# Performance work log

Hardware: AMD Instinct MI355X
Metric: run time of the kernel (lower is better)

The kernel has to match this reference:

```python
import jax, jax.numpy as jnp
import numpy as np

K = 20
EPS = 1e-5


def _bn(x, g, b):
    # inference-mode BatchNorm with running_mean=0, running_var=1 (fresh init)
    return x * (g / jnp.sqrt(1.0 + EPS)) + b


def _lrelu(x):
    return jax.nn.leaky_relu(x, 0.2)


def _knn(x, k):
    # x: [B,N,D] -> idx [B,N,k] of nearest neighbors (includes self)
    sq = jnp.sum(x * x, axis=-1)                       # [B,N]
    inner = jnp.einsum('bnd,bmd->bnm', x, x)           # [B,N,N]
    dist = sq[:, :, None] - 2.0 * inner + sq[:, None, :]
    _, idx = jax.lax.top_k(-dist, k)
    return idx


def _edge_feat(x, k):
    # x: [B,N,D] -> [B,N,k,2D] = concat(neighbor - center, center)
    idx = _knn(x, k)
    nbr = jax.vmap(lambda xb, ib: xb[ib])(x, idx)      # [B,N,k,D]
    ctr = jnp.broadcast_to(x[:, :, None, :], nbr.shape)
    return jnp.concatenate([nbr - ctr, ctr], axis=-1)


def _edge_conv(x, W, g, b, k):
    # conv1x1 (no bias) + BN + LeakyReLU + max over neighbors
    f = _edge_feat(x, k)                               # [B,N,k,2D]
    h = jnp.einsum('bnkc,oc->bnko', f, W)
    return jnp.max(_lrelu(_bn(h, g, b)), axis=2)       # [B,N,out]


def setup_inputs() -> dict:
    key = jax.random.key(0)
    ks = jax.random.split(key, 12)
    B, N = 8, 4096
    num_classes = 5
    r = lambda k_, shape: jax.random.normal(k_, shape, jnp.float32) * 0.1
    return {
        'xyz': jax.random.normal(ks[0], (B, N, 3), jnp.float32),
        'W1': r(ks[1], (64, 6)),   'g1': jnp.ones((64,), jnp.float32),  'b1': jnp.zeros((64,), jnp.float32),
        'W2': r(ks[2], (64, 128)), 'g2': jnp.ones((64,), jnp.float32),  'b2': jnp.zeros((64,), jnp.float32),
        'W3': r(ks[3], (64, 128)), 'g3': jnp.ones((64,), jnp.float32),  'b3': jnp.zeros((64,), jnp.float32),
        'W4': r(ks[4], (128, 128)),'g4': jnp.ones((128,), jnp.float32), 'b4': jnp.zeros((128,), jnp.float32),
        'W5': r(ks[5], (1024, 320)),'g5': jnp.ones((1024,), jnp.float32),'b5': jnp.zeros((1024,), jnp.float32),
        'Wl1': r(ks[6], (512, 2048)),'g6': jnp.ones((512,), jnp.float32),'b6': jnp.zeros((512,), jnp.float32),
        'Wl2': r(ks[7], (256, 512)), 'bl2': jnp.zeros((256,), jnp.float32),
        'g7': jnp.ones((256,), jnp.float32), 'b7': jnp.zeros((256,), jnp.float32),
        'Wl3': r(ks[8], (num_classes, 256)), 'bl3': jnp.zeros((num_classes,), jnp.float32),
    }


def reference(xyz, W1, g1, b1, W2, g2, b2, W3, g3, b3, W4, g4, b4,
              W5, g5, b5, Wl1, g6, b6, Wl2, bl2, g7, b7, Wl3, bl3):
    B, N, _ = xyz.shape
    k = min(K, N - 1)
    x1 = _edge_conv(xyz, W1, g1, b1, k)                # [B,N,64]
    x2 = _edge_conv(x1, W2, g2, b2, k)                 # [B,N,64]
    x3 = _edge_conv(x2, W3, g3, b3, k)                 # [B,N,64]
    x4 = _edge_conv(x3, W4, g4, b4, k)                 # [B,N,128]
    xc = jnp.concatenate([x1, x2, x3, x4], axis=-1)    # [B,N,320]
    h = _lrelu(_bn(jnp.einsum('bnc,oc->bno', xc, W5), g5, b5))  # [B,N,1024]
    gmax = jnp.max(h, axis=1)
    gavg = jnp.mean(h, axis=1)
    gfeat = jnp.concatenate([gmax, gavg], axis=-1)     # [B,2048]
    y = _lrelu(_bn(gfeat @ Wl1.T, g6, b6))             # dropout = identity (eval)
    y = _lrelu(_bn(y @ Wl2.T + bl2, g7, b7))
    y = y @ Wl3.T + bl3                                # [B,num_classes]
    return jnp.broadcast_to(y[:, None, :], (B, N, y.shape[-1]))
```

## Files before the change

kernel.cpp:

```cpp
#include <hip/hip_runtime.h>


constexpr int NB  = 8;
constexpr int NPT = 4096;
constexpr int KNB = 20;
constexpr int CAP = 128;

typedef _Float16 half8 __attribute__((ext_vector_type(8)));
typedef float f32x4 __attribute__((ext_vector_type(4)));

__device__ __forceinline__ unsigned int fmono(float f) {
  unsigned int u = __float_as_uint(f);
  return u ^ ((unsigned int)(((int)u) >> 31) | 0x80000000u);
}

__device__ __attribute__((noinline)) unsigned long long compact_row(
    int row, int n, int lane) {
  extern __shared__ char smem[];
  unsigned long long* buf = (unsigned long long*)smem + (size_t)row * CAP;
  const unsigned long long INFK = ~0ull;
  unsigned long long a = (lane < n) ? buf[lane] : INFK;
  unsigned long long c = (lane + 64 < n) ? buf[lane + 64] : INFK;
#pragma unroll
  for (int k = 2; k <= 64; k <<= 1) {
#pragma unroll
    for (int j = k >> 1; j > 0; j >>= 1) {
      const bool tm = (((lane & k) == 0) == ((lane & j) == 0));
      const unsigned long long oa = __shfl_xor(a, j, 64);
      a = ((a < oa) == tm) ? a : oa;
      const unsigned long long oc = __shfl_xor(c, j, 64);
      c = ((c < oc) == tm) ? oc : c;
    }
  }
  unsigned long long m = a < c ? a : c;
#pragma unroll
  for (int j = 32; j > 0; j >>= 1) {
    const unsigned long long o = __shfl_xor(m, j, 64);
    const bool low = (lane & j) == 0;
    m = ((m < o) == low) ? m : o;
  }
  return m;
}

__device__ __forceinline__ void sel4(unsigned long long k0,
                                     unsigned long long k1,
                                     unsigned long long k2,
                                     unsigned long long k3, int base_r,
                                     int quad, int lane, unsigned int below,
                                     unsigned long long& tau, int& cnt) {
  extern __shared__ char smem[];
  unsigned long long* bufB = (unsigned long long*)smem;
#pragma unroll 1
  for (int attempt = 0; attempt < 2; ++attempt) {
    const unsigned long long m0 = __ballot(k0 < tau);
    const unsigned long long m1 = __ballot(k1 < tau);
    const unsigned long long m2 = __ballot(k2 < tau);
    const unsigned long long m3 = __ballot(k3 < tau);
    if ((m0 | m1 | m2 | m3) == 0ull) return;
    const int sh = quad * 16;
    const unsigned int s0 = (unsigned int)(m0 >> sh) & 0xFFFFu;
    const unsigned int s1 = (unsigned int)(m1 >> sh) & 0xFFFFu;
    const unsigned int s2 = (unsigned int)(m2 >> sh) & 0xFFFFu;
    const unsigned int s3 = (unsigned int)(m3 >> sh) & 0xFFFFu;
    const int tot = __popc(s0) + __popc(s1) + __popc(s2) + __popc(s3);
    const unsigned long long needm = __ballot(cnt + tot > CAP);
    if (needm != 0ull && attempt == 0) {
#pragma unroll
      for (int q = 0; q < 4; ++q) {
        if ((needm >> (q * 16)) & 1ull) {
          const int nq = __shfl(cnt, q * 16, 64);
          const unsigned long long sv = compact_row(base_r + q * 4, nq, lane);
          const unsigned long long t19 = __shfl(sv, 19, 64);
          if (lane < 20) bufB[(size_t)(base_r + q * 4) * CAP + lane] = sv;
          if (quad == q) { tau = t19; cnt = 20; }
        }
      }
      continue;
    }
    int pos = cnt + __popc(s0 & below) + __popc(s1 & below) +
              __popc(s2 & below) + __popc(s3 & below);
    unsigned long long* bp = bufB + (size_t)(base_r + quad * 4) * CAP;
    if (k0 < tau) { bp[pos] = k0; ++pos; }
    if (k1 < tau) { bp[pos] = k1; ++pos; }
    if (k2 < tau) { bp[pos] = k2; ++pos; }
    if (k3 < tau) { bp[pos] = k3; }
    cnt += tot;
    return;
  }
}

__global__ __launch_bounds__(256) void cvt_xyz(const float* __restrict__ xyz,
                                               float* __restrict__ x0) {
  const int t = blockIdx.x * 256 + threadIdx.x;
  float4 v;
  v.x = xyz[t * 3 + 0];
  v.y = xyz[t * 3 + 1];
  v.z = xyz[t * 3 + 2];
  v.w = 0.0f;
  *(float4*)(x0 + (size_t)t * 4) = v;
}

__global__ __launch_bounds__(256) void sqsplit(const float* __restrict__ x,
                                               float* __restrict__ sqo,
                                               unsigned short* __restrict__ xhi,
                                               unsigned short* __restrict__ xlo) {
  const int t = blockIdx.x * 256 + threadIdx.x;
  const int p = t >> 2, c = t & 3;
  const float* src = x + (size_t)p * 64 + c * 16;
  float s = 0.0f;
  unsigned short hb[16], lb[16];
#pragma unroll
  for (int e = 0; e < 16; e += 4) {
    const float4 v = *(const float4*)(src + e);
    const float vv[4] = {v.x, v.y, v.z, v.w};
#pragma unroll
    for (int u = 0; u < 4; ++u) {
      const float f = vv[u];
      s = fmaf(f, f, s);
      const _Float16 h = (_Float16)f;
      const _Float16 l = (_Float16)(f - (float)h);
      hb[e + u] = __builtin_bit_cast(unsigned short, h);
      lb[e + u] = __builtin_bit_cast(unsigned short, l);
    }
  }
  unsigned short* dh = xhi + (size_t)p * 64 + c * 16;
  unsigned short* dl = xlo + (size_t)p * 64 + c * 16;
  *(uint4*)dh = *(uint4*)hb;
  *(uint4*)(dh + 8) = *(uint4*)(hb + 8);
  *(uint4*)dl = *(uint4*)lb;
  *(uint4*)(dl + 8) = *(uint4*)(lb + 8);
  s += __shfl_xor(s, 1, 64);
  s += __shfl_xor(s, 2, 64);
  if (c == 0) sqo[p] = s;
}

__global__ __launch_bounds__(256, 2) void knn3(const float* __restrict__ x0,
                                               int* __restrict__ idxout) {
  const int bid = blockIdx.x;
  const int b = bid & 7;
  const int i0 = (bid >> 3) * 64;
  const int tid = threadIdx.x, w = tid >> 6, lane = tid & 63;
  const int l15 = lane & 15, quad = lane >> 4;
  const unsigned int below = (1u << l15) - 1u;
  const float* xb = x0 + (size_t)b * (NPT * 4);

  float xix[4], xiy[4], xiz[4];
#pragma unroll
  for (int r = 0; r < 4; ++r) {
    const float4 v =
        *(const float4*)(xb + (size_t)(i0 + w * 16 + quad * 4 + r) * 4);
    xix[r] = v.x;
    xiy[r] = v.y;
    xiz[r] = v.z;
  }

  unsigned long long tau[4] = {~0ull, ~0ull, ~0ull, ~0ull};
  int cnt[4] = {0, 0, 0, 0};

  for (int jt = 0; jt < NPT / 64; ++jt) {
    const int j0 = jt * 64;
    float4 xj[4];
#pragma unroll
    for (int nj = 0; nj < 4; ++nj)
      xj[nj] = *(const float4*)(xb + (size_t)(j0 + nj * 16 + l15) * 4);
#pragma unroll
    for (int r = 0; r < 4; ++r) {
      unsigned long long k[4];
#pragma unroll
      for (int nj = 0; nj < 4; ++nj) {
        const float dx = xj[nj].x - xix[r];
        const float dy = xj[nj].y - xiy[r];
        const float dz = xj[nj].z - xiz[r];
        const float dd = fmaf(dx, dx, fmaf(dy, dy, dz * dz));
        k[nj] = ((unsigned long long)fmono(dd) << 32) |
                (unsigned int)(j0 + nj * 16 + l15);
      }
      sel4(k[0], k[1], k[2], k[3], w * 16 + r, quad, lane, below, tau[r],
           cnt[r]);
    }
  }
#pragma unroll 1
  for (int rw = 0; rw < 16; ++rw) {
    const int q = rw >> 2, r = rw & 3;
    const int nq = __shfl(cnt[r], q * 16, 64);
    const unsigned long long sv = compact_row(w * 16 + rw, nq, lane);
    const int i = i0 + w * 16 + rw;
    if (lane < 20)
      idxout[((size_t)(b * NPT + i)) * KNB + lane] = (int)(unsigned int)sv;
  }
}

__global__ __launch_bounds__(256, 2) void knn_mfma(
    const unsigned short* __restrict__ xhi16,
    const unsigned short* __restrict__ xlo16,
    const float* __restrict__ sqn, int* __restrict__ idxout) {
  const int bid = blockIdx.x;
  const int b = bid & 7;
  const int i0 = (bid >> 3) * 64;
  const int tid = threadIdx.x, w = tid >> 6, lane = tid & 63;
  const int l15 = lane & 15, quad = lane >> 4;
  const unsigned int below = (1u << l15) - 1u;

  const half8* Hb = (const half8*)(xhi16 + (size_t)b * NPT * 64);
  const half8* Lb = (const half8*)(xlo16 + (size_t)b * NPT * 64);
  const float* sqb = sqn + b * NPT;

  const int ia = i0 + w * 16 + l15;
  const half8 ah0 = Hb[(size_t)ia * 8 + quad];
  const half8 ah1 = Hb[(size_t)ia * 8 + 4 + quad];
  const half8 al0 = Lb[(size_t)ia * 8 + quad];
  const half8 al1 = Lb[(size_t)ia * 8 + 4 + quad];

  unsigned long long tau[4] = {~0ull, ~0ull, ~0ull, ~0ull};
  int cnt[4] = {0, 0, 0, 0};

  for (int jt = 0; jt < NPT / 64; ++jt) {
    const int j0 = jt * 64;
    float sq4[4];
#pragma unroll
    for (int nj = 0; nj < 4; ++nj) sq4[nj] = sqb[j0 + nj * 16 + l15];
    f32x4 acc[4];
#pragma unroll
    for (int nj = 0; nj < 4; ++nj) {
      const int jb = j0 + nj * 16 + l15;
      const half8 bh0 = Hb[(size_t)jb * 8 + quad];
      const half8 bh1 = Hb[(size_t)jb * 8 + 4 + quad];
      const half8 bl0 = Lb[(size_t)jb * 8 + quad];
      const half8 bl1 = Lb[(size_t)jb * 8 + 4 + quad];
      f32x4 a = {0.0f, 0.0f, 0.0f, 0.0f};
      a = __builtin_amdgcn_mfma_f32_16x16x32_f16(al0, bh0, a, 0, 0, 0);
      a = __builtin_amdgcn_mfma_f32_16x16x32_f16(al1, bh1, a, 0, 0, 0);
      a = __builtin_amdgcn_mfma_f32_16x16x32_f16(ah0, bl0, a, 0, 0, 0);
      a = __builtin_amdgcn_mfma_f32_16x16x32_f16(ah1, bl1, a, 0, 0, 0);
      a = __builtin_amdgcn_mfma_f32_16x16x32_f16(ah0, bh0, a, 0, 0, 0);
      a = __builtin_amdgcn_mfma_f32_16x16x32_f16(ah1, bh1, a, 0, 0, 0);
      acc[nj] = a;
    }
#pragma unroll
    for (int r = 0; r < 4; ++r) {
      unsigned long long k[4];
#pragma unroll
      for (int nj = 0; nj < 4; ++nj) {
        const float dd = fmaf(-2.0f, acc[nj][r], sq4[nj]);
        k[nj] = ((unsigned long long)fmono(dd) << 32) |
                (unsigned int)(j0 + nj * 16 + l15);
      }
      sel4(k[0], k[1], k[2], k[3], w * 16 + r, quad, lane, below, tau[r],
           cnt[r]);
    }
  }
#pragma unroll 1
  for (int rw = 0; rw < 16; ++rw) {
    const int q = rw >> 2, r = rw & 3;
    const int nq = __shfl(cnt[r], q * 16, 64);
    const unsigned long long sv = compact_row(w * 16 + rw, nq, lane);
    const int i = i0 + w * 16 + rw;
    if (lane < 20)
      idxout[((size_t)(b * NPT + i)) * KNB + lane] = (int)(unsigned int)sv;
  }
}

__global__ __launch_bounds__(256) void featg3(const float* __restrict__ x0,
                                              const float* __restrict__ W,
                                              float* __restrict__ Y) {
  const int lane = threadIdx.x & 63;
  const int p0 = (blockIdx.x * 4 + (threadIdx.x >> 6)) * 4;
  const float* wr = W + lane * 6;
  const float w0 = wr[0], w1 = wr[1], w2 = wr[2];
#pragma unroll
  for (int r = 0; r < 4; ++r) {
    const float4 v = *(const float4*)(x0 + (size_t)(p0 + r) * 4);
    Y[(size_t)(p0 + r) * 64 + lane] = w0 * v.x + w1 * v.y + w2 * v.z;
  }
}

__global__ __launch_bounds__(256) void featg64(const float* __restrict__ X,
                                               const float* __restrict__ W,
                                               int co, float* __restrict__ Y) {
  __shared__ float Xt[64][68];
  __shared__ float Wt[64][68];
  const int tid = threadIdx.x;
  const int n0 = blockIdx.x * 64;
  const int pc = tid & 63, dg = tid >> 6;
#pragma unroll
  for (int rep = 0; rep < 4; ++rep) {
    const int d0 = dg * 16 + rep * 4;
    const float4 xv = *(const float4*)(X + (size_t)(n0 + pc) * 64 + d0);
    Xt[d0 + 0][pc] = xv.x; Xt[d0 + 1][pc] = xv.y;
    Xt[d0 + 2][pc] = xv.z; Xt[d0 + 3][pc] = xv.w;
    const float4 wv = *(const float4*)(W + (size_t)(co + pc) * 128 + d0);
    Wt[d0 + 0][pc] = wv.x; Wt[d0 + 1][pc] = wv.y;
    Wt[d0 + 2][pc] = wv.z; Wt[d0 + 3][pc] = wv.w;
  }
  __syncthreads();
  const int c0 = (tid & 15) * 4, p0 = (tid >> 4) * 4;
  float acc[4][4];
#pragma unroll
  for (int i = 0; i < 4; ++i)
#pragma unroll
    for (int j = 0; j < 4; ++j) acc[i][j] = 0.0f;
#pragma unroll 4
  for (int d = 0; d < 64; ++d) {
    const float4 xa = *(const float4*)&Xt[d][p0];
    const float4 wc = *(const float4*)&Wt[d][c0];
    const float xr[4] = {xa.x, xa.y, xa.z, xa.w};
    const float wr[4] = {wc.x, wc.y, wc.z, wc.w};
#pragma unroll
    for (int i = 0; i < 4; ++i)
#pragma unroll
      for (int j = 0; j < 4; ++j) acc[i][j] = fmaf(xr[i], wr[j], acc[i][j]);
  }
#pragma unroll
  for (int i = 0; i < 4; ++i) {
    float4 o;
    o.x = acc[i][0]; o.y = acc[i][1]; o.z = acc[i][2]; o.w = acc[i][3];
    *(float4*)(Y + (size_t)(n0 + p0 + i) * 64 + c0) = o;
  }
}

template <int DIN, int DS, int COUT>
__global__ __launch_bounds__(256) void gather_edge(
    const float* __restrict__ x, const float* __restrict__ Y,
    const int* __restrict__ idx, const float* __restrict__ W,
    const float* __restrict__ g, const float* __restrict__ bia,
    float* __restrict__ out, int co) {
  const int lane = threadIdx.x & 63;
  const int wglob = blockIdx.x * 4 + (threadIdx.x >> 6);
  const int b = wglob >> 12;
  const int c = co + lane;

  const float* wrow = W + (size_t)c * (2 * DIN);
  const float* xi = x + (size_t)wglob * DS;
  float Dv = 0.0f;
  if constexpr (DIN == 3) {
    const float4 v = *(const float4*)xi;
    Dv = (wrow[3] - wrow[0]) * v.x + (wrow[4] - wrow[1]) * v.y +
         (wrow[5] - wrow[2]) * v.z;
  } else {
#pragma unroll
    for (int d0 = 0; d0 < DIN; d0 += 4) {
      const float4 wa4 = *(const float4*)(wrow + d0);
      const float4 wb4 = *(const float4*)(wrow + DIN + d0);
      const float4 v = *(const float4*)(xi + d0);
      Dv += (wb4.x - wa4.x) * v.x + (wb4.y - wa4.y) * v.y +
            (wb4.z - wa4.z) * v.z + (wb4.w - wa4.w) * v.w;
    }
  }
  const float invs = 1.0f / sqrtf(1.0f + 1e-5f);
  const float s = g[c] * invs;
  const float base = fmaf(s, Dv, bia[c]);

  const int* ip = idx + (size_t)wglob * KNB;
  const int jv = ip[lane < KNB ? lane : 0];
  const float* Yb = Y + (((size_t)b) << 12) * 64;
  float m = -3.0e38f;
#pragma unroll
  for (int k = 0; k < KNB; ++k) {
    const int j = __shfl(jv, k, 64);
    const float yv = Yb[(size_t)j * 64 + lane];
    float v = fmaf(s, yv, base);
    v = v > 0.0f ? v : 0.2f * v;
    m = fmaxf(m, v);
  }
  out[(size_t)wglob * COUT + c] = m;
}

__global__ __launch_bounds__(256) void conv5_kernel(
    const float* __restrict__ x1, const float* __restrict__ x2,
    const float* __restrict__ x3, const float* __restrict__ x4,
    const float* __restrict__ W5, const float* __restrict__ g5,
    const float* __restrict__ b5, float* __restrict__ pmax,
    float* __restrict__ psum) {
  __shared__ float xcT[320][32];
  __shared__ float wT[8][256];
  const int nb = blockIdx.x, cb = blockIdx.y, b = blockIdx.z;
  const int tid = threadIdx.x;
  const int n0 = nb * 32;

#pragma unroll
  for (int p = 0; p < 10; ++p) {
    const int q = tid + p * 256;
    const int nloc = q / 80;
    const int kg = (q % 80) * 4;
    const float* src;
    int koff;
    if (kg < 64)       { src = x1 + ((size_t)(b * NPT + n0 + nloc)) * 64;  koff = kg; }
    else if (kg < 128) { src = x2 + ((size_t)(b * NPT + n0 + nloc)) * 64;  koff = kg - 64; }
    else if (kg < 192) { src = x3 + ((size_t)(b * NPT + n0 + nloc)) * 64;  koff = kg - 128; }
    else               { src = x4 + ((size_t)(b * NPT + n0 + nloc)) * 128; koff = kg - 192; }
    const float4 v = *(const float4*)(src + koff);
    xcT[kg + 0][nloc] = v.x; xcT[kg + 1][nloc] = v.y;
    xcT[kg + 2][nloc] = v.z; xcT[kg + 3][nloc] = v.w;
  }

  const int cg = tid >> 2, ng = tid & 3;
  const int c0 = cg * 4, n0t = ng * 8;
  float acc[4][8];
#pragma unroll
  for (int r = 0; r < 4; ++r)
#pragma unroll
    for (int e = 0; e < 8; ++e) acc[r][e] = 0.0f;

  const float* wbase = W5 + (size_t)(cb * 256 + tid) * 320;
  float4 wA = *(const float4*)(wbase);
  float4 wB = *(const float4*)(wbase + 4);

  for (int kt = 0; kt < 40; ++kt) {
    __syncthreads();
    wT[0][tid] = wA.x; wT[1][tid] = wA.y; wT[2][tid] = wA.z; wT[3][tid] = wA.w;
    wT[4][tid] = wB.x; wT[5][tid] = wB.y; wT[6][tid] = wB.z; wT[7][tid] = wB.w;
    const int kn = (kt + 1 < 40) ? kt + 1 : 39;
    float4 nA = *(const float4*)(wbase + kn * 8);
    float4 nB = *(const float4*)(wbase + kn * 8 + 4);
    __syncthreads();
#pragma unroll
    for (int kk = 0; kk < 8; ++kk) {
      const float4 w4 = *(const float4*)&wT[kk][c0];
      const float4 xa = *(const float4*)&xcT[kt * 8 + kk][n0t];
      const float4 xb4 = *(const float4*)&xcT[kt * 8 + kk][n0t + 4];
      const float wr[4] = {w4.x, w4.y, w4.z, w4.w};
      const float xr[8] = {xa.x, xa.y, xa.z, xa.w, xb4.x, xb4.y, xb4.z, xb4.w};
#pragma unroll
      for (int r = 0; r < 4; ++r)
#pragma unroll
        for (int e = 0; e < 8; ++e) acc[r][e] = fmaf(wr[r], xr[e], acc[r][e]);
    }
    wA = nA; wB = nB;
  }

  const float invs = 1.0f / sqrtf(1.0f + 1e-5f);
#pragma unroll
  for (int r = 0; r < 4; ++r) {
    const int cglob = cb * 256 + c0 + r;
    const float s = g5[cglob] * invs;
    const float bb = b5[cglob];
    float mx = -3.0e38f, sm = 0.0f;
#pragma unroll
    for (int e = 0; e < 8; ++e) {
      float v = fmaf(s, acc[r][e], bb);
      v = v > 0.0f ? v : 0.2f * v;
      mx = fmaxf(mx, v);
      sm += v;
    }
    mx = fmaxf(mx, __shfl_xor(mx, 1, 64));
    mx = fmaxf(mx, __shfl_xor(mx, 2, 64));
    sm += __shfl_xor(sm, 1, 64);
    sm += __shfl_xor(sm, 2, 64);
    if (ng == 0) {
      pmax[((size_t)b * 1024 + cglob) * 128 + nb] = mx;
      psum[((size_t)b * 1024 + cglob) * 128 + nb] = sm;
    }
  }
}

__global__ __launch_bounds__(256) void reduce5(const float* __restrict__ pmax,
                                               const float* __restrict__ psum,
                                               float* __restrict__ gfeat) {
  const int t = blockIdx.x * 256 + threadIdx.x;
  const int b = t >> 10, c = t & 1023;
  const float* pm = pmax + (size_t)t * 128;
  const float* ps = psum + (size_t)t * 128;
  float mx = -3.0e38f, sm = 0.0f;
  for (int i = 0; i < 128; i += 4) {
    const float4 v = *(const float4*)(pm + i);
    mx = fmaxf(mx, fmaxf(fmaxf(v.x, v.y), fmaxf(v.z, v.w)));
    const float4 u = *(const float4*)(ps + i);
    sm += (u.x + u.y) + (u.z + u.w);
  }
  gfeat[b * 2048 + c] = mx;
  gfeat[b * 2048 + 1024 + c] = sm * (1.0f / 4096.0f);
}

__global__ __launch_bounds__(256) void head1(const float* __restrict__ gfeat,
                                             const float* __restrict__ Wl1,
                                             const float* __restrict__ g6,
                                             const float* __restrict__ b6,
                                             float* __restrict__ y1g) {
  __shared__ float gf[2048];
  __shared__ float red[256];
  const int tid = threadIdx.x;
  const int cb = blockIdx.x, b = blockIdx.y;
  const float4* gsrc = (const float4*)(gfeat + b * 2048);
  for (int p = tid; p < 512; p += 256) ((float4*)gf)[p] = gsrc[p];
  __syncthreads();
  const int cl = cb * 64 + (tid >> 2);
  const int q = tid & 3;
  const float* wr = Wl1 + (size_t)cl * 2048 + q * 512;
  const float* gq = gf + q * 512;
  float acc = 0.0f;
  for (int k0 = 0; k0 < 512; k0 += 8) {
    const float4 w0 = *(const float4*)(wr + k0);
    const float4 w1 = *(const float4*)(wr + k0 + 4);
    acc = fmaf(w0.x, gq[k0 + 0], acc); acc = fmaf(w0.y, gq[k0 + 1], acc);
    acc = fmaf(w0.z, gq[k0 + 2], acc); acc = fmaf(w0.w, gq[k0 + 3], acc);
    acc = fmaf(w1.x, gq[k0 + 4], acc); acc = fmaf(w1.y, gq[k0 + 5], acc);
    acc = fmaf(w1.z, gq[k0 + 6], acc); acc = fmaf(w1.w, gq[k0 + 7], acc);
  }
  red[tid] = acc;
  __syncthreads();
  if (q == 0) {
    float v = red[tid] + red[tid + 1] + red[tid + 2] + red[tid + 3];
    const float invs = 1.0f / sqrtf(1.0f + 1e-5f);
    v = fmaf(g6[cl] * invs, v, b6[cl]);
    v = v > 0.0f ? v : 0.2f * v;
    y1g[b * 512 + cl] = v;
  }
}

__global__ __launch_bounds__(256) void head2(
    const float* __restrict__ y1g, const float* __restrict__ Wl2,
    const float* __restrict__ bl2, const float* __restrict__ g7,
    const float* __restrict__ b7, const float* __restrict__ Wl3,
    const float* __restrict__ bl3, float* __restrict__ out) {
  __shared__ float y1s[512];
  __shared__ float y2s[256];
  __shared__ float y3s[5];
// ... 28 lines not shown
  }
  __syncthreads();
  for (int e = t; e < NPT * 5; e += 256)
    out[(size_t)b * (NPT * 5) + e] = y3s[e % 5];
}

extern "C" void kernel_launch(void* const* d_in, const int* in_sizes, int n_in,
                              void* d_out, int out_size, void* d_ws, size_t ws_size,
                              hipStream_t stream) {
  (void)in_sizes; (void)n_in; (void)out_size;
  const float* xyz = (const float*)d_in[0];
  const float* W1  = (const float*)d_in[1];
  const float* g1  = (const float*)d_in[2];
  const float* b1  = (const float*)d_in[3];
  const float* W2  = (const float*)d_in[4];
  const float* g2  = (const float*)d_in[5];
  const float* b2  = (const float*)d_in[6];
  const float* W3  = (const float*)d_in[7];
  const float* g3  = (const float*)d_in[8];
  const float* b3  = (const float*)d_in[9];
  const float* W4  = (const float*)d_in[10];
  const float* g4  = (const float*)d_in[11];
  const float* b4  = (const float*)d_in[12];
  const float* W5  = (const float*)d_in[13];
  const float* g5  = (const float*)d_in[14];
  const float* b5  = (const float*)d_in[15];
  const float* Wl1 = (const float*)d_in[16];
  const float* g6  = (const float*)d_in[17];
  const float* b6  = (const float*)d_in[18];
  const float* Wl2 = (const float*)d_in[19];
  const float* bl2 = (const float*)d_in[20];
  const float* g7  = (const float*)d_in[21];
  const float* b7  = (const float*)d_in[22];
  const float* Wl3 = (const float*)d_in[23];
  const float* bl3 = (const float*)d_in[24];

  char* ws = (char*)d_ws;
  float* x0    = (float*)(ws + 0);
  float* x1    = (float*)(ws + 524288);
  float* x2    = (float*)(ws + 8912896);
  float* x3    = (float*)(ws + 17301504);
  float* x4    = (float*)(ws + 25690112);
  float* sqb   = (float*)(ws + 42467328);
  int*   idxb  = (int*)  (ws + 42598400);
  float* pmx   = (float*)(ws + 45219840);
  float* psm   = (float*)(ws + 49414144);
  float* gfeat = (float*)(ws + 53608448);
  float* y1g   = (float*)(ws + 53673984);
  if (ws_size < 53690368) return;

  unsigned short* xhi = (unsigned short*)pmx;
  unsigned short* xlo = (unsigned short*)psm;
  float* Yb = pmx;

  cvt_xyz<<<128, 256, 0, stream>>>(xyz, x0);

  knn3<<<512, 256, 65536, stream>>>(x0, idxb);
  featg3<<<2048, 256, 0, stream>>>(x0, W1, Yb);
  gather_edge<3, 4, 64><<<8192, 256, 0, stream>>>(x0, Yb, idxb, W1, g1, b1, x1, 0);

  sqsplit<<<512, 256, 0, stream>>>(x1, sqb, xhi, xlo);
  knn_mfma<<<512, 256, 65536, stream>>>(xhi, xlo, sqb, idxb);
  featg64<<<512, 256, 0, stream>>>(x1, W2, 0, Yb);
  gather_edge<64, 64, 64><<<8192, 256, 0, stream>>>(x1, Yb, idxb, W2, g2, b2, x2, 0);

  sqsplit<<<512, 256, 0, stream>>>(x2, sqb, xhi, xlo);
  knn_mfma<<<512, 256, 65536, stream>>>(xhi, xlo, sqb, idxb);
  featg64<<<512, 256, 0, stream>>>(x2, W3, 0, Yb);
  gather_edge<64, 64, 64><<<8192, 256, 0, stream>>>(x2, Yb, idxb, W3, g3, b3, x3, 0);

  sqsplit<<<512, 256, 0, stream>>>(x3, sqb, xhi, xlo);
  knn_mfma<<<512, 256, 65536, stream>>>(xhi, xlo, sqb, idxb);
  featg64<<<512, 256, 0, stream>>>(x3, W4, 0, Yb);
  gather_edge<64, 64, 128><<<8192, 256, 0, stream>>>(x3, Yb, idxb, W4, g4, b4, x4, 0);
  featg64<<<512, 256, 0, stream>>>(x3, W4, 64, Yb);
  gather_edge<64, 64, 128><<<8192, 256, 0, stream>>>(x3, Yb, idxb, W4, g4, b4, x4, 64);

  conv5_kernel<<<dim3(128, 4, 8), 256, 0, stream>>>(x1, x2, x3, x4, W5, g5, b5, pmx, psm);
  reduce5<<<32, 256, 0, stream>>>(pmx, psm, gfeat);
  head1<<<dim3(8, 8), 256, 0, stream>>>(gfeat, Wl1, g6, b6, y1g);
  head2<<<8, 256, 0, stream>>>(y1g, Wl2, bl2, g7, b7, Wl3, bl3, (float*)d_out);
}
```

Baseline: 2.316 ms.

## Prefetch next KNN tile in registers and interleave batch index in block mapping

Both KNN kernels now software-pipeline the candidate-point loads: the next 64-point tile (coordinates, or fp16 hi/lo halves plus squared norms) is loaded into registers while the current tile's distances and selection run. The intent is to hide global load latency behind the selection work. The featg3, featg64 and gather_edge kernels remap blockIdx so that consecutive blocks cycle across batches, which changes the L2/cache locality pattern. The compaction loop in sel4 is no longer unrolled, to reduce code size. The prefetch uses more VGPRs (16 half8 values in the MFMA kernel), which could lower occupancy under launch_bounds(256,2).

```diff
diff --git a/kernel.cpp b/kernel.cpp
--- a/kernel.cpp
+++ b/kernel.cpp
@@ -65,7 +65,7 @@
     const int tot = __popc(s0) + __popc(s1) + __popc(s2) + __popc(s3);
     const unsigned long long needm = __ballot(cnt + tot > CAP);
     if (needm != 0ull && attempt == 0) {
-#pragma unroll
+#pragma unroll 1
       for (int q = 0; q < 4; ++q) {
         if ((needm >> (q * 16)) & 1ull) {
           const int nq = __shfl(cnt, q * 16, 64);
@@ -157,20 +157,28 @@
   unsigned long long tau[4] = {~0ull, ~0ull, ~0ull, ~0ull};
   int cnt[4] = {0, 0, 0, 0};
 
+  float4 cj[4];
+#pragma unroll
+  for (int nj = 0; nj < 4; ++nj)
+    cj[nj] = *(const float4*)(xb + (size_t)(nj * 16 + l15) * 4);
+
   for (int jt = 0; jt < NPT / 64; ++jt) {
     const int j0 = jt * 64;
-    float4 xj[4];
-#pragma unroll
-    for (int nj = 0; nj < 4; ++nj)
-      xj[nj] = *(const float4*)(xb + (size_t)(j0 + nj * 16 + l15) * 4);
+    float4 nj4[4];
+    {
+      const int jn0 = (jt + 1 < NPT / 64 ? jt + 1 : jt) * 64;
+#pragma unroll
+      for (int nj = 0; nj < 4; ++nj)
+        nj4[nj] = *(const float4*)(xb + (size_t)(jn0 + nj * 16 + l15) * 4);
+    }
 #pragma unroll
     for (int r = 0; r < 4; ++r) {
       unsigned long long k[4];
 #pragma unroll
       for (int nj = 0; nj < 4; ++nj) {
-        const float dx = xj[nj].x - xix[r];
-        const float dy = xj[nj].y - xiy[r];
-        const float dz = xj[nj].z - xiz[r];
+        const float dx = cj[nj].x - xix[r];
+        const float dy = cj[nj].y - xiy[r];
+        const float dz = cj[nj].z - xiz[r];
         const float dd = fmaf(dx, dx, fmaf(dy, dy, dz * dz));
         k[nj] = ((unsigned long long)fmono(dd) << 32) |
                 (unsigned int)(j0 + nj * 16 + l15);
@@ -178,6 +186,8 @@
       sel4(k[0], k[1], k[2], k[3], w * 16 + r, quad, lane, below, tau[r],
            cnt[r]);
     }
+#pragma unroll
+    for (int nj = 0; nj < 4; ++nj) cj[nj] = nj4[nj];
   }
 #pragma unroll 1
   for (int rw = 0; rw < 16; ++rw) {
@@ -214,26 +224,44 @@
   unsigned long long tau[4] = {~0ull, ~0ull, ~0ull, ~0ull};
   int cnt[4] = {0, 0, 0, 0};
 
+  half8 cb[16];
+  float sqc[4];
+#pragma unroll
+  for (int nj = 0; nj < 4; ++nj) {
+    const int jb = nj * 16 + l15;
+    cb[nj * 4 + 0] = Hb[(size_t)jb * 8 + quad];
+    cb[nj * 4 + 1] = Hb[(size_t)jb * 8 + 4 + quad];
+    cb[nj * 4 + 2] = Lb[(size_t)jb * 8 + quad];
+    cb[nj * 4 + 3] = Lb[(size_t)jb * 8 + 4 + quad];
+    sqc[nj] = sqb[nj * 16 + l15];
+  }
+
   for (int jt = 0; jt < NPT / 64; ++jt) {
     const int j0 = jt * 64;
-    float sq4[4];
-#pragma unroll
-    for (int nj = 0; nj < 4; ++nj) sq4[nj] = sqb[j0 + nj * 16 + l15];
+    half8 nb[16];
+    float sqn4[4];
+    {
+      const int jn0 = (jt + 1 < NPT / 64 ? jt + 1 : jt) * 64;
+#pragma unroll
+      for (int nj = 0; nj < 4; ++nj) {
+        const int jb = jn0 + nj * 16 + l15;
+        nb[nj * 4 + 0] = Hb[(size_t)jb * 8 + quad];
+        nb[nj * 4 + 1] = Hb[(size_t)jb * 8 + 4 + quad];
+        nb[nj * 4 + 2] = Lb[(size_t)jb * 8 + quad];
+        nb[nj * 4 + 3] = Lb[(size_t)jb * 8 + 4 + quad];
+        sqn4[nj] = sqb[jn0 + nj * 16 + l15];
+      }
+    }
     f32x4 acc[4];
 #pragma unroll
     for (int nj = 0; nj < 4; ++nj) {
-      const int jb = j0 + nj * 16 + l15;
-      const half8 bh0 = Hb[(size_t)jb * 8 + quad];
-      const half8 bh1 = Hb[(size_t)jb * 8 + 4 + quad];
-      const half8 bl0 = Lb[(size_t)jb * 8 + quad];
-      const half8 bl1 = Lb[(size_t)jb * 8 + 4 + quad];
       f32x4 a = {0.0f, 0.0f, 0.0f, 0.0f};
-      a = __builtin_amdgcn_mfma_f32_16x16x32_f16(al0, bh0, a, 0, 0, 0);
-      a = __builtin_amdgcn_mfma_f32_16x16x32_f16(al1, bh1, a, 0, 0, 0);
-      a = __builtin_amdgcn_mfma_f32_16x16x32_f16(ah0, bl0, a, 0, 0, 0);
-      a = __builtin_amdgcn_mfma_f32_16x16x32_f16(ah1, bl1, a, 0, 0, 0);
-      a = __builtin_amdgcn_mfma_f32_16x16x32_f16(ah0, bh0, a, 0, 0, 0);
-      a = __builtin_amdgcn_mfma_f32_16x16x32_f16(ah1, bh1, a, 0, 0, 0);
+      a = __builtin_amdgcn_mfma_f32_16x16x32_f16(al0, cb[nj * 4 + 0], a, 0, 0, 0);
+      a = __builtin_amdgcn_mfma_f32_16x16x32_f16(al1, cb[nj * 4 + 1], a, 0, 0, 0);
+      a = __builtin_amdgcn_mfma_f32_16x16x32_f16(ah0, cb[nj * 4 + 2], a, 0, 0, 0);
+      a = __builtin_amdgcn_mfma_f32_16x16x32_f16(ah1, cb[nj * 4 + 3], a, 0, 0, 0);
+      a = __builtin_amdgcn_mfma_f32_16x16x32_f16(ah0, cb[nj * 4 + 0], a, 0, 0, 0);
+      a = __builtin_amdgcn_mfma_f32_16x16x32_f16(ah1, cb[nj * 4 + 1], a, 0, 0, 0);
       acc[nj] = a;
     }
 #pragma unroll
@@ -241,13 +269,17 @@
       unsigned long long k[4];
 #pragma unroll
       for (int nj = 0; nj < 4; ++nj) {
-        const float dd = fmaf(-2.0f, acc[nj][r], sq4[nj]);
+        const float dd = fmaf(-2.0f, acc[nj][r], sqc[nj]);
         k[nj] = ((unsigned long long)fmono(dd) << 32) |
                 (unsigned int)(j0 + nj * 16 + l15);
       }
       sel4(k[0], k[1], k[2], k[3], w * 16 + r, quad, lane, below, tau[r],
            cnt[r]);
     }
+#pragma unroll
+    for (int e = 0; e < 16; ++e) cb[e] = nb[e];
+#pragma unroll
+    for (int nj = 0; nj < 4; ++nj) sqc[nj] = sqn4[nj];
   }
 #pragma unroll 1
   for (int rw = 0; rw < 16; ++rw) {
@@ -264,7 +296,9 @@
                                               const float* __restrict__ W,
                                               float* __restrict__ Y) {
   const int lane = threadIdx.x & 63;
-  const int p0 = (blockIdx.x * 4 + (threadIdx.x >> 6)) * 4;
+  const int bid = blockIdx.x;
+  const int p0 =
+      ((bid & 7) << 12) + ((bid >> 3) * 4 + (threadIdx.x >> 6)) * 4;
   const float* wr = W + lane * 6;
   const float w0 = wr[0], w1 = wr[1], w2 = wr[2];
 #pragma unroll
@@ -280,7 +314,8 @@
   __shared__ float Xt[64][68];
   __shared__ float Wt[64][68];
   const int tid = threadIdx.x;
-  const int n0 = blockIdx.x * 64;
+  const int bid = blockIdx.x;
+  const int n0 = ((bid & 7) << 12) + (bid >> 3) * 64;
   const int pc = tid & 63, dg = tid >> 6;
 #pragma unroll
   for (int rep = 0; rep < 4; ++rep) {
@@ -325,7 +360,8 @@
     const float* __restrict__ g, const float* __restrict__ bia,
     float* __restrict__ out, int co) {
   const int lane = threadIdx.x & 63;
-  const int wglob = blockIdx.x * 4 + (threadIdx.x >> 6);
+  const int bid = blockIdx.x;
+  const int wglob = ((bid & 7) << 12) + (bid >> 3) * 4 + (threadIdx.x >> 6);
   const int b = wglob >> 12;
   const int c = co + lane;
 
```

After: 2.258 ms. 2.5% less time.

## Split kNN candidate range across two blocks with shared global threshold and merge

Applied to the files above, without the earlier changes.

Each kNN kernel now processes half of the candidate columns per block, doubling the grid to 1024 blocks with smaller shared buffers (CAP 80) and higher occupancy. Blocks working on the same query rows share a pruning threshold through global atomicMin every 8 tiles, and each writes its partial top-20 to a scratch buffer. A new merge kernel bitonic-sorts the 40 partial candidates into the final indices. Selection is also split into two-key batches, and block-to-point mappings in the feature and gather kernels are interleaved across batches. The aim is to fill more of the GPU and prune sooner, at the cost of extra launches (tau_init, merge), atomics and scratch traffic.

```diff
diff --git a/kernel.cpp b/kernel.cpp
--- a/kernel.cpp
+++ b/kernel.cpp
@@ -4,7 +4,7 @@
 constexpr int NB  = 8;
 constexpr int NPT = 4096;
 constexpr int KNB = 20;
-constexpr int CAP = 128;
+constexpr int CAP = 80;
 
 typedef _Float16 half8 __attribute__((ext_vector_type(8)));
 typedef float f32x4 __attribute__((ext_vector_type(4)));
@@ -42,51 +42,71 @@
   return m;
 }
 
-__device__ __forceinline__ void sel4(unsigned long long k0,
-                                     unsigned long long k1,
-                                     unsigned long long k2,
-                                     unsigned long long k3, int base_r,
-                                     int quad, int lane, unsigned int below,
-                                     unsigned long long& tau, int& cnt) {
+__device__ __forceinline__ void selpair(unsigned long long k0,
+                                        unsigned long long k1, int base_r,
+                                        int quad, int lane, unsigned int below,
+                                        unsigned long long* __restrict__ tauG,
+                                        int gb, unsigned long long& tau,
+                                        int& cnt) {
   extern __shared__ char smem[];
   unsigned long long* bufB = (unsigned long long*)smem;
 #pragma unroll 1
   for (int attempt = 0; attempt < 2; ++attempt) {
     const unsigned long long m0 = __ballot(k0 < tau);
     const unsigned long long m1 = __ballot(k1 < tau);
-    const unsigned long long m2 = __ballot(k2 < tau);
-    const unsigned long long m3 = __ballot(k3 < tau);
-    if ((m0 | m1 | m2 | m3) == 0ull) return;
+    if ((m0 | m1) == 0ull) return;
     const int sh = quad * 16;
     const unsigned int s0 = (unsigned int)(m0 >> sh) & 0xFFFFu;
     const unsigned int s1 = (unsigned int)(m1 >> sh) & 0xFFFFu;
-    const unsigned int s2 = (unsigned int)(m2 >> sh) & 0xFFFFu;
-    const unsigned int s3 = (unsigned int)(m3 >> sh) & 0xFFFFu;
-    const int tot = __popc(s0) + __popc(s1) + __popc(s2) + __popc(s3);
+    const int tot = __popc(s0) + __popc(s1);
     const unsigned long long needm = __ballot(cnt + tot > CAP);
     if (needm != 0ull && attempt == 0) {
-#pragma unroll
+#pragma unroll 1
       for (int q = 0; q < 4; ++q) {
         if ((needm >> (q * 16)) & 1ull) {
+          const int row = base_r + q * 4;
           const int nq = __shfl(cnt, q * 16, 64);
-          const unsigned long long sv = compact_row(base_r + q * 4, nq, lane);
+          const unsigned long long sv = compact_row(row, nq, lane);
           const unsigned long long t19 = __shfl(sv, 19, 64);
-          if (lane < 20) bufB[(size_t)(base_r + q * 4) * CAP + lane] = sv;
-          if (quad == q) { tau = t19; cnt = 20; }
+          if (lane < 20) bufB[(size_t)row * CAP + lane] = sv;
+          if (lane == q * 16) atomicMin(tauG + gb + row, t19);
+          if (quad == q) {
+            tau = tau < t19 ? tau : t19;
+            cnt = 20;
+          }
         }
       }
       continue;
     }
-    int pos = cnt + __popc(s0 & below) + __popc(s1 & below) +
-              __popc(s2 & below) + __popc(s3 & below);
+    int pos = cnt + __popc(s0 & below) + __popc(s1 & below);
     unsigned long long* bp = bufB + (size_t)(base_r + quad * 4) * CAP;
     if (k0 < tau) { bp[pos] = k0; ++pos; }
-    if (k1 < tau) { bp[pos] = k1; ++pos; }
-    if (k2 < tau) { bp[pos] = k2; ++pos; }
-    if (k3 < tau) { bp[pos] = k3; }
+    if (k1 < tau) { bp[pos] = k1; }
     cnt += tot;
     return;
   }
+}
+
+__global__ __launch_bounds__(256) void tau_init(
+    unsigned long long* __restrict__ tauG) {
+  tauG[blockIdx.x * 256 + threadIdx.x] = ~0ull;
+}
+
+__global__ __launch_bounds__(256) void knn_merge(
+    const unsigned long long* __restrict__ part, int* __restrict__ idxout) {
+  const int lane = threadIdx.x & 63;
+  const int p = blockIdx.x * 4 + (threadIdx.x >> 6);
+  unsigned long long a = (lane < 40) ? part[(size_t)p * 40 + lane] : ~0ull;
+#pragma unroll
+  for (int k = 2; k <= 64; k <<= 1) {
+#pragma unroll
+    for (int j = k >> 1; j > 0; j >>= 1) {
+      const bool tm = (((lane & k) == 0) == ((lane & j) == 0));
+      const unsigned long long oa = __shfl_xor(a, j, 64);
+      a = ((a < oa) == tm) ? a : oa;
+    }
+  }
+  if (lane < 20) idxout[(size_t)p * KNB + lane] = (int)(unsigned int)a;
 }
 
 __global__ __launch_bounds__(256) void cvt_xyz(const float* __restrict__ xyz,
@@ -134,14 +154,18 @@
   if (c == 0) sqo[p] = s;
 }
 
-__global__ __launch_bounds__(256, 2) void knn3(const float* __restrict__ x0,
-                                               int* __restrict__ idxout) {
+__global__ __launch_bounds__(256, 4) void knn3(
+    const float* __restrict__ x0, unsigned long long* __restrict__ part,
+    unsigned long long* __restrict__ tauG) {
   const int bid = blockIdx.x;
   const int b = bid & 7;
-  const int i0 = (bid >> 3) * 64;
+  const int tb = bid >> 3;
+  const int i0 = (tb >> 1) * 64;
+  const int jh = tb & 1;
   const int tid = threadIdx.x, w = tid >> 6, lane = tid & 63;
   const int l15 = lane & 15, quad = lane >> 4;
   const unsigned int below = (1u << l15) - 1u;
+  const int gb = b * NPT + i0;
   const float* xb = x0 + (size_t)b * (NPT * 4);
 
   float xix[4], xiy[4], xiz[4];
@@ -157,7 +181,7 @@
   unsigned long long tau[4] = {~0ull, ~0ull, ~0ull, ~0ull};
   int cnt[4] = {0, 0, 0, 0};
 
-  for (int jt = 0; jt < NPT / 64; ++jt) {
+  for (int jt = jh * 32; jt < jh * 32 + 32; ++jt) {
     const int j0 = jt * 64;
     float4 xj[4];
 #pragma unroll
@@ -175,8 +199,20 @@
         k[nj] = ((unsigned long long)fmono(dd) << 32) |
                 (unsigned int)(j0 + nj * 16 + l15);
       }
-      sel4(k[0], k[1], k[2], k[3], w * 16 + r, quad, lane, below, tau[r],
-           cnt[r]);
+      selpair(k[0], k[1], w * 16 + r, quad, lane, below, tauG, gb, tau[r],
+              cnt[r]);
+      selpair(k[2], k[3], w * 16 + r, quad, lane, below, tauG, gb, tau[r],
+              cnt[r]);
+    }
+    if ((jt & 7) == 7) {
+#pragma unroll
+      for (int r = 0; r < 4; ++r) {
+        unsigned long long got = tau[r];
+        if (l15 == 0)
+          got = atomicMin(tauG + gb + w * 16 + quad * 4 + r, tau[r]);
+        const unsigned long long o = __shfl(got, quad << 4, 64);
+        tau[r] = tau[r] < o ? tau[r] : o;
+      }
     }
   }
 #pragma unroll 1
@@ -184,22 +220,25 @@
     const int q = rw >> 2, r = rw & 3;
     const int nq = __shfl(cnt[r], q * 16, 64);
     const unsigned long long sv = compact_row(w * 16 + rw, nq, lane);
-    const int i = i0 + w * 16 + rw;
     if (lane < 20)
-      idxout[((size_t)(b * NPT + i)) * KNB + lane] = (int)(unsigned int)sv;
-  }
-}
-
-__global__ __launch_bounds__(256, 2) void knn_mfma(
+      part[((size_t)(gb + w * 16 + rw)) * 40 + jh * 20 + lane] = sv;
+  }
+}
+
+__global__ __launch_bounds__(256, 4) void knn_mfma(
     const unsigned short* __restrict__ xhi16,
-    const unsigned short* __restrict__ xlo16,
-    const float* __restrict__ sqn, int* __restrict__ idxout) {
+    const unsigned short* __restrict__ xlo16, const float* __restrict__ sqn,
+    unsigned long long* __restrict__ part,
+    unsigned long long* __restrict__ tauG) {
   const int bid = blockIdx.x;
   const int b = bid & 7;
-  const int i0 = (bid >> 3) * 64;
+  const int tb = bid >> 3;
+  const int i0 = (tb >> 1) * 64;
+  const int jh = tb & 1;
   const int tid = threadIdx.x, w = tid >> 6, lane = tid & 63;
   const int l15 = lane & 15, quad = lane >> 4;
   const unsigned int below = (1u << l15) - 1u;
+  const int gb = b * NPT + i0;
 
   const half8* Hb = (const half8*)(xhi16 + (size_t)b * NPT * 64);
   const half8* Lb = (const half8*)(xlo16 + (size_t)b * NPT * 64);
@@ -214,7 +253,7 @@
   unsigned long long tau[4] = {~0ull, ~0ull, ~0ull, ~0ull};
   int cnt[4] = {0, 0, 0, 0};
 
-  for (int jt = 0; jt < NPT / 64; ++jt) {
+  for (int jt = jh * 32; jt < jh * 32 + 32; ++jt) {
     const int j0 = jt * 64;
     float sq4[4];
 #pragma unroll
@@ -245,8 +284,20 @@
         k[nj] = ((unsigned long long)fmono(dd) << 32) |
                 (unsigned int)(j0 + nj * 16 + l15);
       }
-      sel4(k[0], k[1], k[2], k[3], w * 16 + r, quad, lane, below, tau[r],
-           cnt[r]);
+      selpair(k[0], k[1], w * 16 + r, quad, lane, below, tauG, gb, tau[r],
+              cnt[r]);
+      selpair(k[2], k[3], w * 16 + r, quad, lane, below, tauG, gb, tau[r],
+              cnt[r]);
+    }
+    if ((jt & 7) == 7) {
+#pragma unroll
+      for (int r = 0; r < 4; ++r) {
+        unsigned long long got = tau[r];
+        if (l15 == 0)
+          got = atomicMin(tauG + gb + w * 16 + quad * 4 + r, tau[r]);
+        const unsigned long long o = __shfl(got, quad << 4, 64);
+        tau[r] = tau[r] < o ? tau[r] : o;
+      }
     }
   }
 #pragma unroll 1
@@ -254,9 +305,8 @@
     const int q = rw >> 2, r = rw & 3;
     const int nq = __shfl(cnt[r], q * 16, 64);
     const unsigned long long sv = compact_row(w * 16 + rw, nq, lane);
-    const int i = i0 + w * 16 + rw;
     if (lane < 20)
-      idxout[((size_t)(b * NPT + i)) * KNB + lane] = (int)(unsigned int)sv;
+      part[((size_t)(gb + w * 16 + rw)) * 40 + jh * 20 + lane] = sv;
   }
 }
 
@@ -264,7 +314,9 @@
                                               const float* __restrict__ W,
                                               float* __restrict__ Y) {
   const int lane = threadIdx.x & 63;
-  const int p0 = (blockIdx.x * 4 + (threadIdx.x >> 6)) * 4;
+  const int bid = blockIdx.x;
+  const int p0 =
+      ((bid & 7) << 12) + ((bid >> 3) * 4 + (threadIdx.x >> 6)) * 4;
   const float* wr = W + lane * 6;
   const float w0 = wr[0], w1 = wr[1], w2 = wr[2];
 #pragma unroll
@@ -280,7 +332,8 @@
   __shared__ float Xt[64][68];
   __shared__ float Wt[64][68];
   const int tid = threadIdx.x;
-  const int n0 = blockIdx.x * 64;
+  const int bid = blockIdx.x;
+  const int n0 = ((bid & 7) << 12) + (bid >> 3) * 64;
   const int pc = tid & 63, dg = tid >> 6;
 #pragma unroll
   for (int rep = 0; rep < 4; ++rep) {
@@ -325,7 +378,8 @@
     const float* __restrict__ g, const float* __restrict__ bia,
     float* __restrict__ out, int co) {
   const int lane = threadIdx.x & 63;
-  const int wglob = blockIdx.x * 4 + (threadIdx.x >> 6);
+  const int bid = blockIdx.x;
+  const int wglob = ((bid & 7) << 12) + (bid >> 3) * 4 + (threadIdx.x >> 6);
   const int b = wglob >> 12;
   const int c = co + lane;
 
@@ -596,25 +650,35 @@
   unsigned short* xhi = (unsigned short*)pmx;
   unsigned short* xlo = (unsigned short*)psm;
   float* Yb = pmx;
+  unsigned long long* part = (unsigned long long*)x4;
+  unsigned long long* tauG = (unsigned long long*)((char*)x4 + 10485760);
 
   cvt_xyz<<<128, 256, 0, stream>>>(xyz, x0);
 
-  knn3<<<512, 256, 65536, stream>>>(x0, idxb);
+  tau_init<<<128, 256, 0, stream>>>(tauG);
+  knn3<<<1024, 256, 40960, stream>>>(x0, part, tauG);
+  knn_merge<<<8192, 256, 0, stream>>>(part, idxb);
   featg3<<<2048, 256, 0, stream>>>(x0, W1, Yb);
   gather_edge<3, 4, 64><<<8192, 256, 0, stream>>>(x0, Yb, idxb, W1, g1, b1, x1, 0);
 
   sqsplit<<<512, 256, 0, stream>>>(x1, sqb, xhi, xlo);
-  knn_mfma<<<512, 256, 65536, stream>>>(xhi, xlo, sqb, idxb);
+  tau_init<<<128, 256, 0, stream>>>(tauG);
+  knn_mfma<<<1024, 256, 40960, stream>>>(xhi, xlo, sqb, part, tauG);
+  knn_merge<<<8192, 256, 0, stream>>>(part, idxb);
   featg64<<<512, 256, 0, stream>>>(x1, W2, 0, Yb);
   gather_edge<64, 64, 64><<<8192, 256, 0, stream>>>(x1, Yb, idxb, W2, g2, b2, x2, 0);
 
   sqsplit<<<512, 256, 0, stream>>>(x2, sqb, xhi, xlo);
-  knn_mfma<<<512, 256, 65536, stream>>>(xhi, xlo, sqb, idxb);
+  tau_init<<<128, 256, 0, stream>>>(tauG);
+  knn_mfma<<<1024, 256, 40960, stream>>>(xhi, xlo, sqb, part, tauG);
+  knn_merge<<<8192, 256, 0, stream>>>(part, idxb);
   featg64<<<512, 256, 0, stream>>>(x2, W3, 0, Yb);
   gather_edge<64, 64, 64><<<8192, 256, 0, stream>>>(x2, Yb, idxb, W3, g3, b3, x3, 0);
 
   sqsplit<<<512, 256, 0, stream>>>(x3, sqb, xhi, xlo);
-  knn_mfma<<<512, 256, 65536, stream>>>(xhi, xlo, sqb, idxb);
+  tau_init<<<128, 256, 0, stream>>>(tauG);
+  knn_mfma<<<1024, 256, 40960, stream>>>(xhi, xlo, sqb, part, tauG);
+  knn_merge<<<8192, 256, 0, stream>>>(part, idxb);
   featg64<<<512, 256, 0, stream>>>(x3, W4, 0, Yb);
   gather_edge<64, 64, 128><<<8192, 256, 0, stream>>>(x3, Yb, idxb, W4, g4, b4, x4, 0);
   featg64<<<512, 256, 0, stream>>>(x3, W4, 64, Yb);
```

Measured after the change: 2.657 ms. +14.7%, slower.

## Port conv5 to split-fp16 MFMA and remap block indices across batches

Applied to the files above, without the earlier changes.

Rewrites the conv5 1x1 convolution from FP32 FMA tiles to MFMA 16x16x32 fp16 instructions. Each operand is split into a high and a low fp16 part, and three MFMAs per tile approximate FP32 accuracy. A new splitW5 kernel pre-splits the weights into a reused buffer, and the partial max/sum layout shrinks to 64 tiles per channel, with reduce5 adjusted to match. Block indices in featg3, featg64 and gather_edge are interleaved across batches, which changes the memory access locality, and one compaction loop is de-unrolled to reduce code size. The split-fp16 trick adds conversion work and gives slightly lower precision than true FP32.

```diff
diff --git a/kernel.cpp b/kernel.cpp
--- a/kernel.cpp
+++ b/kernel.cpp
@@ -65,7 +65,7 @@
     const int tot = __popc(s0) + __popc(s1) + __popc(s2) + __popc(s3);
     const unsigned long long needm = __ballot(cnt + tot > CAP);
     if (needm != 0ull && attempt == 0) {
-#pragma unroll
+#pragma unroll 1
       for (int q = 0; q < 4; ++q) {
         if ((needm >> (q * 16)) & 1ull) {
           const int nq = __shfl(cnt, q * 16, 64);
@@ -264,7 +264,9 @@
                                               const float* __restrict__ W,
                                               float* __restrict__ Y) {
   const int lane = threadIdx.x & 63;
-  const int p0 = (blockIdx.x * 4 + (threadIdx.x >> 6)) * 4;
+  const int bid = blockIdx.x;
+  const int p0 =
+      ((bid & 7) << 12) + ((bid >> 3) * 4 + (threadIdx.x >> 6)) * 4;
   const float* wr = W + lane * 6;
   const float w0 = wr[0], w1 = wr[1], w2 = wr[2];
 #pragma unroll
@@ -280,7 +282,8 @@
   __shared__ float Xt[64][68];
   __shared__ float Wt[64][68];
   const int tid = threadIdx.x;
-  const int n0 = blockIdx.x * 64;
+  const int bid = blockIdx.x;
+  const int n0 = ((bid & 7) << 12) + (bid >> 3) * 64;
   const int pc = tid & 63, dg = tid >> 6;
 #pragma unroll
   for (int rep = 0; rep < 4; ++rep) {
@@ -325,7 +328,8 @@
     const float* __restrict__ g, const float* __restrict__ bia,
     float* __restrict__ out, int co) {
   const int lane = threadIdx.x & 63;
-  const int wglob = blockIdx.x * 4 + (threadIdx.x >> 6);
+  const int bid = blockIdx.x;
+  const int wglob = ((bid & 7) << 12) + (bid >> 3) * 4 + (threadIdx.x >> 6);
   const int b = wglob >> 12;
   const int c = co + lane;
 
@@ -365,90 +369,108 @@
   out[(size_t)wglob * COUT + c] = m;
 }
 
-__global__ __launch_bounds__(256) void conv5_kernel(
+__global__ __launch_bounds__(256) void splitW5(
+    const float* __restrict__ W5, unsigned short* __restrict__ whi,
+    unsigned short* __restrict__ wlo) {
+  const int t = blockIdx.x * 256 + threadIdx.x;
+  const float4 v = *(const float4*)(W5 + (size_t)t * 4);
+  const float vv[4] = {v.x, v.y, v.z, v.w};
+  unsigned short hb[4], lb[4];
+#pragma unroll
+  for (int u = 0; u < 4; ++u) {
+    const _Float16 h = (_Float16)vv[u];
+    const _Float16 l = (_Float16)(vv[u] - (float)h);
+    hb[u] = __builtin_bit_cast(unsigned short, h);
+    lb[u] = __builtin_bit_cast(unsigned short, l);
+  }
+  *(uint2*)(whi + (size_t)t * 4) = *(uint2*)hb;
+  *(uint2*)(wlo + (size_t)t * 4) = *(uint2*)lb;
+}
+
+__global__ __launch_bounds__(256) void conv5_mfma(
     const float* __restrict__ x1, const float* __restrict__ x2,
     const float* __restrict__ x3, const float* __restrict__ x4,
-    const float* __restrict__ W5, const float* __restrict__ g5,
+    const unsigned short* __restrict__ whi,
+    const unsigned short* __restrict__ wlo, const float* __restrict__ g5,
     const float* __restrict__ b5, float* __restrict__ pmax,
     float* __restrict__ psum) {
-  __shared__ float xcT[320][32];
-  __shared__ float wT[8][256];
-  const int nb = blockIdx.x, cb = blockIdx.y, b = blockIdx.z;
-  const int tid = threadIdx.x;
-  const int n0 = nb * 32;
-
-#pragma unroll
-  for (int p = 0; p < 10; ++p) {
-    const int q = tid + p * 256;
-    const int nloc = q / 80;
-    const int kg = (q % 80) * 4;
+  __shared__ __align__(16) unsigned short xh[64][40];
+  __shared__ __align__(16) unsigned short xl[64][40];
+  const int nt = blockIdx.x, ct = blockIdx.y, b = blockIdx.z;
+  const int tid = threadIdx.x, wv = tid >> 6, lane = tid & 63;
+  const int l15 = lane & 15, quad = lane >> 4;
+  const int n0 = nt * 64, c0 = ct * 64;
+
+  const int nl = tid >> 2;
+  const int kg = (tid & 3) * 8;
+
+  f32x4 acc[4];
+#pragma unroll
+  for (int nj = 0; nj < 4; ++nj) acc[nj] = {0.0f, 0.0f, 0.0f, 0.0f};
+
+  const int ca = c0 + wv * 16 + l15;
+
+  for (int kt = 0; kt < 10; ++kt) {
+    __syncthreads();
+    const int kbase = kt * 32;
     const float* src;
     int koff;
-    if (kg < 64)       { src = x1 + ((size_t)(b * NPT + n0 + nloc)) * 64;  koff = kg; }
-    else if (kg < 128) { src = x2 + ((size_t)(b * NPT + n0 + nloc)) * 64;  koff = kg - 64; }
-    else if (kg < 192) { src = x3 + ((size_t)(b * NPT + n0 + nloc)) * 64;  koff = kg - 128; }
-    else               { src = x4 + ((size_t)(b * NPT + n0 + nloc)) * 128; koff = kg - 192; }
-    const float4 v = *(const float4*)(src + koff);
-    xcT[kg + 0][nloc] = v.x; xcT[kg + 1][nloc] = v.y;
-    xcT[kg + 2][nloc] = v.z; xcT[kg + 3][nloc] = v.w;
-  }
-
-  const int cg = tid >> 2, ng = tid & 3;
-  const int c0 = cg * 4, n0t = ng * 8;
-  float acc[4][8];
-#pragma unroll
-  for (int r = 0; r < 4; ++r)
-#pragma unroll
-    for (int e = 0; e < 8; ++e) acc[r][e] = 0.0f;
-
-  const float* wbase = W5 + (size_t)(cb * 256 + tid) * 320;
-  float4 wA = *(const float4*)(wbase);
-  float4 wB = *(const float4*)(wbase + 4);
-
-  for (int kt = 0; kt < 40; ++kt) {
+    if (kbase < 64)       { src = x1 + ((size_t)(b * NPT + n0 + nl)) * 64;  koff = kbase; }
+    else if (kbase < 128) { src = x2 + ((size_t)(b * NPT + n0 + nl)) * 64;  koff = kbase - 64; }
+    else if (kbase < 192) { src = x3 + ((size_t)(b * NPT + n0 + nl)) * 64;  koff = kbase - 128; }
+    else                  { src = x4 + ((size_t)(b * NPT + n0 + nl)) * 128; koff = kbase - 192; }
+    const float4 v0 = *(const float4*)(src + koff + kg);
+    const float4 v1 = *(const float4*)(src + koff + kg + 4);
+    const float vv[8] = {v0.x, v0.y, v0.z, v0.w, v1.x, v1.y, v1.z, v1.w};
+    unsigned short hb[8], lb[8];
+#pragma unroll
+    for (int u = 0; u < 8; ++u) {
+      const _Float16 h = (_Float16)vv[u];
+      const _Float16 l = (_Float16)(vv[u] - (float)h);
+      hb[u] = __builtin_bit_cast(unsigned short, h);
+      lb[u] = __builtin_bit_cast(unsigned short, l);
+    }
+    *(uint4*)&xh[nl][kg] = *(uint4*)hb;
+    *(uint4*)&xl[nl][kg] = *(uint4*)lb;
     __syncthreads();
-    wT[0][tid] = wA.x; wT[1][tid] = wA.y; wT[2][tid] = wA.z; wT[3][tid] = wA.w;
-    wT[4][tid] = wB.x; wT[5][tid] = wB.y; wT[6][tid] = wB.z; wT[7][tid] = wB.w;
-    const int kn = (kt + 1 < 40) ? kt + 1 : 39;
-    float4 nA = *(const float4*)(wbase + kn * 8);
-    float4 nB = *(const float4*)(wbase + kn * 8 + 4);
-    __syncthreads();
-#pragma unroll
-    for (int kk = 0; kk < 8; ++kk) {
-      const float4 w4 = *(const float4*)&wT[kk][c0];
-      const float4 xa = *(const float4*)&xcT[kt * 8 + kk][n0t];
-      const float4 xb4 = *(const float4*)&xcT[kt * 8 + kk][n0t + 4];
-      const float wr[4] = {w4.x, w4.y, w4.z, w4.w};
-      const float xr[8] = {xa.x, xa.y, xa.z, xa.w, xb4.x, xb4.y, xb4.z, xb4.w};
-#pragma unroll
-      for (int r = 0; r < 4; ++r)
-#pragma unroll
-        for (int e = 0; e < 8; ++e) acc[r][e] = fmaf(wr[r], xr[e], acc[r][e]);
-    }
-    wA = nA; wB = nB;
+    const half8 wh =
+        *(const half8*)(whi + (size_t)ca * 320 + kbase + quad * 8);
+    const half8 wl =
+        *(const half8*)(wlo + (size_t)ca * 320 + kbase + quad * 8);
+#pragma unroll
+    for (int nj = 0; nj < 4; ++nj) {
+      const half8 bh = *(const half8*)&xh[nj * 16 + l15][quad * 8];
+      const half8 bl = *(const half8*)&xl[nj * 16 + l15][quad * 8];
+      f32x4 a = acc[nj];
+      a = __builtin_amdgcn_mfma_f32_16x16x32_f16(wl, bh, a, 0, 0, 0);
+      a = __builtin_amdgcn_mfma_f32_16x16x32_f16(wh, bl, a, 0, 0, 0);
+      a = __builtin_amdgcn_mfma_f32_16x16x32_f16(wh, bh, a, 0, 0, 0);
+      acc[nj] = a;
+    }
   }
 
   const float invs = 1.0f / sqrtf(1.0f + 1e-5f);
 #pragma unroll
   for (int r = 0; r < 4; ++r) {
-    const int cglob = cb * 256 + c0 + r;
-    const float s = g5[cglob] * invs;
-    const float bb = b5[cglob];
+    const int c = c0 + wv * 16 + quad * 4 + r;
+    const float s = g5[c] * invs;
+    const float bb = b5[c];
     float mx = -3.0e38f, sm = 0.0f;
 #pragma unroll
-    for (int e = 0; e < 8; ++e) {
-      float v = fmaf(s, acc[r][e], bb);
+    for (int nj = 0; nj < 4; ++nj) {
+      float v = fmaf(s, acc[nj][r], bb);
       v = v > 0.0f ? v : 0.2f * v;
       mx = fmaxf(mx, v);
       sm += v;
     }
-    mx = fmaxf(mx, __shfl_xor(mx, 1, 64));
-    mx = fmaxf(mx, __shfl_xor(mx, 2, 64));
-    sm += __shfl_xor(sm, 1, 64);
-    sm += __shfl_xor(sm, 2, 64);
-    if (ng == 0) {
-      pmax[((size_t)b * 1024 + cglob) * 128 + nb] = mx;
-      psum[((size_t)b * 1024 + cglob) * 128 + nb] = sm;
+#pragma unroll
+    for (int d = 1; d < 16; d <<= 1) {
+      mx = fmaxf(mx, __shfl_xor(mx, d, 64));
+      sm += __shfl_xor(sm, d, 64);
+    }
+    if (l15 == 0) {
+      pmax[((size_t)b * 1024 + c) * 64 + nt] = mx;
+      psum[((size_t)b * 1024 + c) * 64 + nt] = sm;
     }
   }
 }
@@ -458,10 +480,10 @@
                                                float* __restrict__ gfeat) {
   const int t = blockIdx.x * 256 + threadIdx.x;
   const int b = t >> 10, c = t & 1023;
-  const float* pm = pmax + (size_t)t * 128;
-  const float* ps = psum + (size_t)t * 128;
+  const float* pm = pmax + (size_t)t * 64;
+  const float* ps = psum + (size_t)t * 64;
   float mx = -3.0e38f, sm = 0.0f;
-  for (int i = 0; i < 128; i += 4) {
+  for (int i = 0; i < 64; i += 4) {
     const float4 v = *(const float4*)(pm + i);
     mx = fmaxf(mx, fmaxf(fmaxf(v.x, v.y), fmaxf(v.z, v.w)));
     const float4 u = *(const float4*)(ps + i);
@@ -596,6 +618,8 @@
   unsigned short* xhi = (unsigned short*)pmx;
   unsigned short* xlo = (unsigned short*)psm;
   float* Yb = pmx;
+  unsigned short* whi = (unsigned short*)idxb;
+  unsigned short* wlo = (unsigned short*)idxb + 327680;
 
   cvt_xyz<<<128, 256, 0, stream>>>(xyz, x0);
 
@@ -620,7 +644,9 @@
   featg64<<<512, 256, 0, stream>>>(x3, W4, 64, Yb);
   gather_edge<64, 64, 128><<<8192, 256, 0, stream>>>(x3, Yb, idxb, W4, g4, b4, x4, 64);
 
-  conv5_kernel<<<dim3(128, 4, 8), 256, 0, stream>>>(x1, x2, x3, x4, W5, g5, b5, pmx, psm);
+  splitW5<<<320, 256, 0, stream>>>(W5, whi, wlo);
+  conv5_mfma<<<dim3(64, 16, 8), 256, 0, stream>>>(x1, x2, x3, x4, whi, wlo,
+                                                  g5, b5, pmx, psm);
   reduce5<<<32, 256, 0, stream>>>(pmx, psm, gfeat);
   head1<<<dim3(8, 8), 256, 0, stream>>>(gfeat, Wl1, g6, b6, y1g);
   head2<<<8, 256, 0, stream>>>(y1g, Wl2, bl2, g7, b7, Wl3, bl3, (float*)d_out);
```

Result: faster. 2.258 ms (-2.5%).
